# Kernel optimization log

Measured on AMD Instinct MI355X. Metric: run time of the kernel, lower is better.

The kernel has to match this reference:

```python
import jax, jax.numpy as jnp
import numpy as np

D_MODEL = 96
D_STATE = 16
D_INNER = 192   # expand * d_model
DT_RANK = 6     # ceil(96/16)
D_DEPTH_OUT = 1024  # (64/2)*(64/2)
BATCH, HH, WW = 2, 64, 64


def silu(v):
    return v * jax.nn.sigmoid(v)


def setup_inputs() -> dict:
    key = jax.random.key(0)
    ks = jax.random.split(key, 10)
    f = jnp.float32
    x = jax.random.normal(ks[0], (BATCH, HH, WW, D_MODEL), f)
    in_proj_w = jax.random.normal(ks[1], (2 * D_INNER, D_MODEL), f) * 0.02
    conv2d_w = jax.random.normal(ks[2], (D_INNER, 1, 3, 3), f) * 0.1  # depthwise, groups=D_INNER
    conv2d_b = jnp.zeros((D_INNER,), f)
    depth_conv_w = jax.random.normal(ks[3], (D_INNER, 1, 3, 3), f) * 0.1  # depthwise, stride 2
    depth_conv_b = jnp.zeros((D_INNER,), f)
    depth_fc_w = jax.random.normal(ks[4], (D_INNER, D_DEPTH_OUT), f) * 0.02
    depth_fc_b = jnp.zeros((D_INNER,), f)
    x_proj_w = jax.random.normal(ks[5], (DT_RANK + 2 * D_STATE, D_INNER), f) * 0.02
    dt_init_std = DT_RANK ** (-0.5)
    dt_projs_w = jax.random.uniform(ks[6], (D_INNER, DT_RANK), f, -dt_init_std, dt_init_std)
    # inverse-softplus of dt ~ U(log 1e-3, log 0.1)
    dt = jnp.exp(jax.random.uniform(ks[7], (D_INNER,), f) * (np.log(0.1) - np.log(0.001)) + np.log(0.001))
    dt = jnp.clip(dt, 1e-4, None)
    dt_projs_b = dt + jnp.log(-jnp.expm1(-dt))
    A_logs = jnp.log(jnp.tile(jnp.arange(1, D_STATE + 1, dtype=f)[None, :], (D_INNER, 1)))
    Ds = jnp.ones((D_INNER,), f)
    out_norm_w = jnp.ones((D_INNER,), f)
    out_norm_b = jnp.zeros((D_INNER,), f)
    out_proj_w = jax.random.normal(ks[8], (D_MODEL, D_INNER), f) * 0.02
    return dict(x=x, in_proj_w=in_proj_w, conv2d_w=conv2d_w, conv2d_b=conv2d_b,
                depth_conv_w=depth_conv_w, depth_conv_b=depth_conv_b,
                depth_fc_w=depth_fc_w, depth_fc_b=depth_fc_b, x_proj_w=x_proj_w,
                dt_projs_w=dt_projs_w, dt_projs_b=dt_projs_b, A_logs=A_logs, Ds=Ds,
                out_norm_w=out_norm_w, out_norm_b=out_norm_b, out_proj_w=out_proj_w)


def _selective_scan(u, delta, A, Bm, Cm, D, delta_bias):
    # u, delta: [B, D, L]; A: [D, N]; Bm, Cm: [B, N, L]; D: [D]; delta_bias: [D]
    delta = jax.nn.softplus(delta + delta_bias[None, :, None])
    dA = jnp.exp(jnp.einsum('bdl,dn->lbdn', delta, A))          # [L,B,D,N]
    dBu = jnp.einsum('bdl,bnl,bdl->lbdn', delta, Bm, u)          # [L,B,D,N]
    Ct = jnp.transpose(Cm, (2, 0, 1))                            # [L,B,N]
    h0 = jnp.zeros(dA.shape[1:], u.dtype)

    def step(h, inp):
        a, b, c = inp
        h = a * h + b                                            # S6 recurrence
        return h, jnp.einsum('bdn,bn->bd', h, c)

    _, ys = jax.lax.scan(step, h0, (dA, dBu, Ct))                # ys: [L,B,D]
    y = jnp.transpose(ys, (1, 2, 0))                             # [B,D,L]
    return y + D[None, :, None] * u


def _forward(x, in_proj_w, conv2d_w, conv2d_b, depth_conv_w, depth_conv_b,
             depth_fc_w, depth_fc_b, x_proj_w, dt_projs_w, dt_projs_b,
             A_logs, Ds, out_norm_w, out_norm_b, out_proj_w):
    B, H, W, _ = x.shape
    Di, N, R = D_INNER, D_STATE, DT_RANK
    dn = ('NCHW', 'OIHW', 'NCHW')
    xz = x @ in_proj_w.T
    x1, z = jnp.split(xz, 2, axis=-1)
    xc = jnp.transpose(x1, (0, 3, 1, 2))                         # [B,Di,H,W]
    xc = jax.lax.conv_general_dilated(xc, conv2d_w, (1, 1), [(1, 1), (1, 1)],
                                      dimension_numbers=dn, feature_group_count=Di)
    xc = silu(xc + conv2d_b[None, :, None, None])
    dxc = jax.lax.conv_general_dilated(xc, depth_conv_w, (2, 2), [(1, 1), (1, 1)],
                                       dimension_numbers=dn, feature_group_count=Di)
    dxc = dxc + depth_conv_b[None, :, None, None]                # [B,Di,H/2,W/2]
    dx = dxc.reshape(B, Di, -1)                                  # [B,Di,1024]
    dx = dx @ depth_fc_w.T + depth_fc_b                          # [B,Di,Di]
    dx = silu(jnp.transpose(dx, (0, 2, 1)))                      # [B,Di,CC], CC=Di
    L = H * W
    CC = dx.shape[-1]
    xs = jnp.concatenate([dx, xc.reshape(B, Di, L)], axis=-1)    # mode='head': [B,Di,LL]
    x_dbl = jnp.einsum('bdl,cd->bcl', xs, x_proj_w)
    dts, Bm, Cm = x_dbl[:, :R], x_dbl[:, R:R + N], x_dbl[:, R + N:]
    dts = jnp.einsum('brl,dr->bdl', dts, dt_projs_w)
    A = -jnp.exp(A_logs)
    y = _selective_scan(xs, dts, A, Bm, Cm, Ds, dt_projs_b)
    y = y[..., CC:]                                              # drop depth tokens (head mode)
    y = jnp.transpose(y, (0, 2, 1)).reshape(B, H, W, Di)
    mu = jnp.mean(y, axis=-1, keepdims=True)
    var = jnp.var(y, axis=-1, keepdims=True)
    y = (y - mu) * jax.lax.rsqrt(var + 1e-5) * out_norm_w + out_norm_b
    y = y * silu(z)
    return y @ out_proj_w.T


def reference(x, in_proj_w, conv2d_w, conv2d_b, depth_conv_w, depth_conv_b,
              depth_fc_w, depth_fc_b, x_proj_w, dt_projs_w, dt_projs_b,
              A_logs, Ds, out_norm_w, out_norm_b, out_proj_w):
    return _forward(x, in_proj_w, conv2d_w, conv2d_b, depth_conv_w, depth_conv_b,
                    depth_fc_w, depth_fc_b, x_proj_w, dt_projs_w, dt_projs_b,
                    A_logs, Ds, out_norm_w, out_norm_b, out_proj_w)
```

## Files before the change

kernel.cpp:

```cpp
#include <hip/hip_runtime.h>
#include <hip/hip_bf16.h>

typedef __hip_bfloat16 bf16;

#define BATCH 2
#define DM 96
#define DI 192
#define LSP 4096
#define LD 192
#define LTOT 4288
#define NST 16
#define RK 6
#define DFC 1024
#define CLEN 64
#define NCH 67
#define XR 16

__device__ __forceinline__ float b2f(bf16 v) { return __bfloat162float(v); }
__device__ __forceinline__ float silu_f(float x) { return x / (1.f + __expf(-x)); }
__device__ __forceinline__ float softplus_f(float x) { return x > 20.f ? x : log1pf(__expf(x)); }

__device__ __forceinline__ int is_f32(const void* alog) {
    return ((const unsigned int*)alog)[0] == 0u;
}
__device__ __forceinline__ float LDI(const void* p, int i, int f32m) {
    return f32m ? ((const float*)p)[i] : __bfloat162float(((const bf16*)p)[i]);
}
__device__ __forceinline__ void unpack2(unsigned int u, float* o) {
    o[0] = __uint_as_float(u << 16);
    o[1] = __uint_as_float(u & 0xffff0000u);
}

__global__ __launch_bounds__(768) void k_inproj(const void* __restrict__ x, const void* __restrict__ ipw,
                                                const void* __restrict__ alog,
                                                float* __restrict__ x1, float* __restrict__ z) {
    __shared__ uint4 sxr[384];
    const int f32m = is_f32(alog);
    int t = threadIdx.x;
    int col = t >> 1;
    int kh = t & 1;
    int row0 = blockIdx.x * 16;
    float wr[48];
    if (f32m) {
        const float4* wp = (const float4*)((const float*)ipw + col * 96 + kh * 48);
        #pragma unroll
        for (int i = 0; i < 12; i++) {
            float4 v = wp[i];
            wr[4*i] = v.x; wr[4*i+1] = v.y; wr[4*i+2] = v.z; wr[4*i+3] = v.w;
        }
        if (t < 384) sxr[t] = ((const uint4*)((const float*)x + row0 * 96))[t];
        __syncthreads();
        for (int r = 0; r < 16; r++) {
            const uint4* xr = &sxr[r * 24 + kh * 12];
            float acc = 0.f;
            #pragma unroll
            for (int i = 0; i < 12; i++) {
                uint4 u = xr[i];
                acc += __uint_as_float(u.x) * wr[4*i]   + __uint_as_float(u.y) * wr[4*i+1]
                     + __uint_as_float(u.z) * wr[4*i+2] + __uint_as_float(u.w) * wr[4*i+3];
            }
            acc += __shfl_xor(acc, 1);
            if (kh == 0) {
                int row = row0 + r;
                if (col < DI) x1[row * DI + col] = acc;
                else          z[row * DI + (col - DI)] = acc;
            }
        }
    } else {
        const uint4* wp = (const uint4*)((const bf16*)ipw + col * 96 + kh * 48);
        #pragma unroll
        for (int i = 0; i < 6; i++) {
            uint4 v = wp[i];
            unpack2(v.x, &wr[8*i]);   unpack2(v.y, &wr[8*i+2]);
            unpack2(v.z, &wr[8*i+4]); unpack2(v.w, &wr[8*i+6]);
        }
        if (t < 192) sxr[t] = ((const uint4*)((const bf16*)x + row0 * 96))[t];
        __syncthreads();
        for (int r = 0; r < 16; r++) {
            const uint4* xr = &sxr[r * 12 + kh * 6];
            float acc = 0.f;
            #pragma unroll
            for (int i = 0; i < 6; i++) {
                uint4 xv = xr[i];
                float xf8[8];
                unpack2(xv.x, &xf8[0]); unpack2(xv.y, &xf8[2]);
                unpack2(xv.z, &xf8[4]); unpack2(xv.w, &xf8[6]);
                #pragma unroll
                for (int j = 0; j < 8; j++) acc += xf8[j] * wr[8*i + j];
            }
            acc += __shfl_xor(acc, 1);
            if (kh == 0) {
                int row = row0 + r;
                if (col < DI) x1[row * DI + col] = acc;
                else          z[row * DI + (col - DI)] = acc;
            }
        }
    }
}

__global__ __launch_bounds__(192) void k_conv1(const float* __restrict__ x1, const void* __restrict__ cw,
                                               const void* __restrict__ cb, float* __restrict__ xs,
                                               const void* __restrict__ alog) {
    const int f32m = is_f32(alog);
    int d = threadIdx.x;
    int blk = blockIdx.x;
    int b = blk >> 12, l = blk & 4095;
    int h = l >> 6, w_ = l & 63;
    float acc = LDI(cb, d, f32m);
    #pragma unroll
    for (int dh = 0; dh < 3; dh++) {
        int hh = h + dh - 1;
        if ((unsigned)hh >= 64u) continue;
        #pragma unroll
        for (int dw = 0; dw < 3; dw++) {
            int ww = w_ + dw - 1;
            if ((unsigned)ww >= 64u) continue;
            acc += x1[((b << 12) + (hh << 6) + ww) * DI + d] * LDI(cw, d * 9 + dh * 3 + dw, f32m);
        }
    }
    xs[(b * LTOT + LD + l) * DI + d] = silu_f(acc);
}

__global__ __launch_bounds__(192) void k_conv2(const float* __restrict__ xs, const void* __restrict__ dw,
                                               const void* __restrict__ db, float* __restrict__ dxc,
                                               const void* __restrict__ alog) {
    const int f32m = is_f32(alog);
    int d = threadIdx.x;
    int blk = blockIdx.x;
    int b = blk >> 10, lp = blk & 1023;
    int hp = lp >> 5, wp = lp & 31;
    float acc = LDI(db, d, f32m);
    #pragma unroll
    for (int dh = 0; dh < 3; dh++) {
        int h = 2 * hp + dh - 1;
        if ((unsigned)h >= 64u) continue;
        #pragma unroll
        for (int dw_ = 0; dw_ < 3; dw_++) {
            int w_ = 2 * wp + dw_ - 1;
            if ((unsigned)w_ >= 64u) continue;
            acc += xs[(b * LTOT + LD + (h << 6) + w_) * DI + d] * LDI(dw, d * 9 + dh * 3 + dw_, f32m);
        }
    }
    dxc[(b * DFC + lp) * DI + d] = acc;
}

__global__ __launch_bounds__(192) void k_dfc(const float* __restrict__ dxc, const void* __restrict__ fw,
                                             float* __restrict__ part, const void* __restrict__ alog) {
    __shared__ float sfw[4 * 128];
    const int f32m = is_f32(alog);
    int t = threadIdx.x;
    int blk = blockIdx.x;
    int p = blk / 96;
    int rem = blk - p * 96;
    int b   = rem / 48;
    int ch0 = (rem % 48) * 4;
    int k0  = p * 128;
    for (int idx = t; idx < 4 * 128; idx += 192)
        sfw[idx] = LDI(fw, (ch0 + (idx >> 7)) * DFC + k0 + (idx & 127), f32m);
    __syncthreads();
    float a0 = 0.f, a1 = 0.f, a2 = 0.f, a3 = 0.f;
    #pragma unroll 8
    for (int k = 0; k < 128; k++) {
        float dv = dxc[(b * DFC + k0 + k) * DI + t];
        a0 += dv * sfw[k];
        a1 += dv * sfw[128 + k];
        a2 += dv * sfw[256 + k];
        a3 += dv * sfw[384 + k];
    }
    int ob = ((p * 2 + b) * 192 + t) * DI + ch0;
    *(float4*)&part[ob] = make_float4(a0, a1, a2, a3);
}

__global__ __launch_bounds__(256) void k_xdbl(const float* __restrict__ xs_r, float* __restrict__ xs_w,
                                              const float* __restrict__ part, const void* __restrict__ fb,
                                              const void* __restrict__ xpw,
                                              float* __restrict__ BCb, float* __restrict__ dts,
                                              const void* __restrict__ alog) {
    __shared__ float sw[38 * 196];
    __shared__ float srow[XR][196];
    const int f32m = is_f32(alog);
    int t = threadIdx.x;
    for (int c = t >> 3; c < 38; c += 32) {
        int seg = (t & 7) * 24;
        for (int k = seg; k < seg + 24; k++) sw[c * 196 + k] = LDI(xpw, c * DI + k, f32m);
    }
    int row0 = blockIdx.x * XR;
    int bb = row0 >= LTOT ? 1 : 0;
    int depth = (row0 - bb * LTOT) < LD;
    for (int idx = t; idx < XR * DI; idx += 256) {
        int row = idx / DI, k = idx - row * DI;
        int grow = row0 + row;
        float v;
        if (depth) {
            int tok = grow - bb * LTOT;
            int o = (bb * 192 + tok) * DI + k;
            v = 0.f;
            #pragma unroll
            for (int p = 0; p < 8; p++) v += part[o + p * 73728];
            v = silu_f(v + LDI(fb, k, f32m));
            xs_w[grow * DI + k] = v;
        } else {
            v = xs_r[grow * DI + k];
        }
        srow[row][k] = v;
    }
    __syncthreads();
    int r = t & 15, cg = t >> 4;
    float a0 = 0.f, a1 = 0.f, a2 = 0.f;
    const float4* w0 = (const float4*)&sw[cg * 196];
    const float4* w1 = (const float4*)&sw[(cg + 16) * 196];
    const float4* w2 = (const float4*)&sw[(cg < 6 ? cg + 32 : cg) * 196];
    const float4* xr = (const float4*)&srow[r][0];
    #pragma unroll 4
    for (int k = 0; k < 48; k++) {
        float4 xv = xr[k], v0 = w0[k], v1 = w1[k], v2 = w2[k];
        a0 += xv.x * v0.x + xv.y * v0.y + xv.z * v0.z + xv.w * v0.w;
        a1 += xv.x * v1.x + xv.y * v1.y + xv.z * v1.z + xv.w * v1.w;
        a2 += xv.x * v2.x + xv.y * v2.y + xv.z * v2.z + xv.w * v2.w;
    }
    int grow = row0 + r;
    if (cg < 6) dts[grow * 6 + cg] = a0;
    else        BCb[grow * 32 + (cg - 6)] = a0;
    BCb[grow * 32 + (cg + 10)] = a1;
    if (cg < 6) BCb[grow * 32 + (cg + 26)] = a2;
}

__device__ __forceinline__ void scan_stage(const float* __restrict__ dts, const float* __restrict__ xs,
                                           const float* __restrict__ BCb, const void* __restrict__ dtw,
                                           const void* __restrict__ dtb, int f32m,
                                           int bL, int l0, int d0, int t,
                                           float* su, float* sbc, float* sdel,
                                           float* sdts, float* sdwb) {
    {
        int e = t * 4;
        int i = e >> 4, dd = e & 15;
        *(float4*)&su[e] = *(const float4*)&xs[(bL + l0 + i) * DI + d0 + dd];
    }
    #pragma unroll
    for (int q = 0; q < 2; q++) {
        int e = (t + q * 256) * 4;
        int i = e >> 5, c = e & 31;
        *(float4*)&sbc[e] = *(const float4*)&BCb[(bL + l0 + i) * 32 + c];
    }
    for (int idx = t; idx < CLEN * RK; idx += 256) sdts[idx] = dts[(bL + l0) * RK + idx];
    if (t < 96)            sdwb[t] = LDI(dtw, (d0 + t / 6) * RK + (t % 6), f32m);
    else if (t < 112)      sdwb[t] = LDI(dtb, d0 + (t - 96), f32m);
    __syncthreads();
    {
        int e = t * 4;
        int i = e >> 4, dl = e & 15;
        #pragma unroll
        for (int q = 0; q < 4; q++) {
            int dlq = dl + q;
            float dv = sdwb[96 + dlq];
            #pragma unroll
            for (int r2 = 0; r2 < RK; r2++) dv += sdts[i * RK + r2] * sdwb[dlq * RK + r2];
            sdel[e + q] = softplus_f(dv);
        }
    }
    __syncthreads();
}

__global__ __launch_bounds__(256) void k_scan1(const float* __restrict__ dts, const float* __restrict__ xs,
                                               const float* __restrict__ BCb, const void* __restrict__ dtw,
                                               const void* __restrict__ dtb, const void* __restrict__ alog,
                                               float* __restrict__ Af, float* __restrict__ hf) {
    __shared__ float su[CLEN * 16];
    __shared__ float sbc[CLEN * 32];
    __shared__ float sdel[CLEN * 16];
    __shared__ float sdts[CLEN * RK];
    __shared__ float sdwb[112];
    const int f32m = is_f32(alog);
    int t = threadIdx.x;
    int beta = blockIdx.x;
    int b = beta / (12 * NCH);
    int rem = beta - b * (12 * NCH);
    int dblk = rem / NCH, ch = rem - dblk * NCH;
    int d0 = dblk * 16, l0 = ch * CLEN;
    int bL = b * LTOT;
    scan_stage(dts, xs, BCb, dtw, dtb, f32m, bL, l0, d0, t, su, sbc, sdel, sdts, sdwb);
    int dloc = t >> 4, n = t & 15;
    int d = d0 + dloc;
    float A = -__expf(LDI(alog, d * NST + n, f32m));
    float h = 0.f, ap = 1.f;
    #pragma unroll 4
    for (int i = 0; i < CLEN; i++) {
        float dt = sdel[(i << 4) | dloc];
        float u  = su[(i << 4) | dloc];
        float Bv = sbc[(i << 5) | n];
        float a = __expf(dt * A);
        h = a * h + dt * Bv * u;
        ap *= a;
    }
    int o = ((b * DI + d) * NCH + ch) * NST + n;
    Af[o] = ap;
    hf[o] = h;
}

__global__ __launch_bounds__(256) void k_scan3(const float* __restrict__ dts, const float* __restrict__ xs,
                                               const float* __restrict__ BCb, const void* __restrict__ dtw,
                                               const void* __restrict__ dtb, const void* __restrict__ alog,
                                               const void* __restrict__ Dsv,
                                               const float* __restrict__ Af, const float* __restrict__ hf,
                                               float* __restrict__ y) {
    __shared__ float su[CLEN * 16];
    __shared__ float sbc[CLEN * 32];
    __shared__ float sdel[CLEN * 16];
    __shared__ float sdts[CLEN * RK];
    __shared__ float sdwb[112];
    const int f32m = is_f32(alog);
    int t = threadIdx.x;
    int beta = blockIdx.x;
    int b = beta / (12 * NCH);
    int rem = beta - b * (12 * NCH);
    int dblk = rem / NCH, ch = rem - dblk * NCH;
    int d0 = dblk * 16, l0 = ch * CLEN;
    int bL = b * LTOT;
    scan_stage(dts, xs, BCb, dtw, dtb, f32m, bL, l0, d0, t, su, sbc, sdel, sdts, sdwb);
    int dloc = t >> 4, n = t & 15;
    int d = d0 + dloc;
    float A = -__expf(LDI(alog, d * NST + n, f32m));
    float Dv = LDI(Dsv, d, f32m);
    int base = ((b * DI + d) * NCH) * NST + n;
    float h = 0.f;
    for (int c = 0; c < ch; c++) {
        int oo = base + c * NST;
        h = Af[oo] * h + hf[oo];
    }
    for (int i = 0; i < CLEN; i++) {
        float dt = sdel[(i << 4) | dloc];
        float u  = su[(i << 4) | dloc];
        float Bv = sbc[(i << 5) | n];
        float Cv = sbc[(i << 5) | 16 | n];
        float a = __expf(dt * A);
        h = a * h + dt * Bv * u;
        float yv = h * Cv;
        #pragma unroll
        for (int m = 8; m; m >>= 1) yv += __shfl_xor(yv, m, 16);
        int l = l0 + i;
        if (n == 0 && l >= LD) y[(b * LSP + (l - LD)) * DI + d] = yv + Dv * u;
    }
}

__global__ __launch_bounds__(384) void k_out(const float* __restrict__ y, const float* __restrict__ z,
                                             const void* __restrict__ nw, const void* __restrict__ nb,
                                             const void* __restrict__ opw, void* __restrict__ out,
                                             const void* __restrict__ alog) {
    __shared__ float sg[2][DI];
    __shared__ float sred[2][2][3];
    const int f32m = is_f32(alog);
    int t = threadIdx.x;
    int m = t >> 2, kh = t & 3;
    float wr[48];
    if (f32m) {
        const float4* wp = (const float4*)((const float*)opw + m * DI + kh * 48);
        #pragma unroll
        for (int i = 0; i < 12; i++) {
            float4 v = wp[i];
            wr[4*i] = v.x; wr[4*i+1] = v.y; wr[4*i+2] = v.z; wr[4*i+3] = v.w;
        }
    } else {
        const uint4* wp = (const uint4*)((const bf16*)opw + m * DI + kh * 48);
        #pragma unroll
        for (int i = 0; i < 6; i++) {
            uint4 v = wp[i];
            unpack2(v.x, &wr[8*i]);   unpack2(v.y, &wr[8*i+2]);
            unpack2(v.z, &wr[8*i+4]); unpack2(v.w, &wr[8*i+6]);
        }
    }
    float nwv = 0.f, nbv = 0.f;
    if (t < DI) { nwv = LDI(nw, t, f32m); nbv = LDI(nb, t, f32m); }
    int wv_ = t >> 6;
    int row0 = blockIdx.x * 16;
    for (int pr = 0; pr < 8; pr++) {
        int r0 = row0 + pr * 2, r1 = r0 + 1;
        float y0 = 0.f, z0 = 0.f, y1 = 0.f, z1 = 0.f;
        if (t < DI) {
            y0 = y[r0 * DI + t]; z0 = z[r0 * DI + t];
            y1 = y[r1 * DI + t]; z1 = z[r1 * DI + t];
            float s0 = y0, q0 = y0 * y0, s1 = y1, q1 = y1 * y1;
            #pragma unroll
            for (int off = 32; off; off >>= 1) {
                s0 += __shfl_xor(s0, off); q0 += __shfl_xor(q0, off);
                s1 += __shfl_xor(s1, off); q1 += __shfl_xor(q1, off);
            }
            if ((t & 63) == 0) {
                sred[0][0][wv_] = s0; sred[0][1][wv_] = q0;
                sred[1][0][wv_] = s1; sred[1][1][wv_] = q1;
            }
        }
        __syncthreads();
        if (t < DI) {
            float S0  = sred[0][0][0] + sred[0][0][1] + sred[0][0][2];
            float Q0  = sred[0][1][0] + sred[0][1][1] + sred[0][1][2];
            float S1  = sred[1][0][0] + sred[1][0][1] + sred[1][0][2];
            float Q1  = sred[1][1][0] + sred[1][1][1] + sred[1][1][2];
            float mu0 = S0 * (1.f / 192.f), var0 = Q0 * (1.f / 192.f) - mu0 * mu0;
            float mu1 = S1 * (1.f / 192.f), var1 = Q1 * (1.f / 192.f) - mu1 * mu1;
            float g0 = (y0 - mu0) * rsqrtf(var0 + 1e-5f) * nwv + nbv;
            g0 *= z0 / (1.f + __expf(-z0));
            float g1 = (y1 - mu1) * rsqrtf(var1 + 1e-5f) * nwv + nbv;
            g1 *= z1 / (1.f + __expf(-z1));
            sg[0][t] = g0;
            sg[1][t] = g1;
        }
        __syncthreads();
        const float* g0p = &sg[0][kh * 48];
        const float* g1p = &sg[1][kh * 48];
        float a0 = 0.f, a1 = 0.f;
        #pragma unroll
        for (int j = 0; j < 48; j++) {
            a0 += g0p[j] * wr[j];
            a1 += g1p[j] * wr[j];
        }
        a0 += __shfl_xor(a0, 1); a0 += __shfl_xor(a0, 2);
        a1 += __shfl_xor(a1, 1); a1 += __shfl_xor(a1, 2);
        if (kh == 0) {
            if (f32m) {
                ((float*)out)[r0 * DM + m] = a0;
                ((float*)out)[r1 * DM + m] = a1;
            } else {
                ((bf16*)out)[r0 * DM + m] = __float2bfloat16(a0);
                ((bf16*)out)[r1 * DM + m] = __float2bfloat16(a1);
            }
        }
    }
}

extern "C" void kernel_launch(void* const* d_in, const int* in_sizes, int n_in,
                              void* d_out, int out_size, void* d_ws, size_t ws_size,
                              hipStream_t stream) {
    (void)in_sizes; (void)n_in; (void)out_size; (void)ws_size;
    const void* x    = d_in[0];
    const void* ipw  = d_in[1];
    const void* c1w  = d_in[2];
    const void* c1b  = d_in[3];
    const void* c2w  = d_in[4];
    const void* c2b  = d_in[5];
    const void* fcw  = d_in[6];
    const void* fcb  = d_in[7];
    const void* xpw  = d_in[8];
    const void* dtw  = d_in[9];
    const void* dtb  = d_in[10];
    const void* alog = d_in[11];
    const void* Dsv  = d_in[12];
    const void* nw   = d_in[13];
    const void* nb   = d_in[14];
    const void* opw  = d_in[15];

    float* ws  = (float*)d_ws;
    float* x1  = ws;
    float* z   = x1  + BATCH * LSP * DI;
    float* xs  = z   + BATCH * LSP * DI;
    float* dxc = xs  + BATCH * LTOT * DI;
    float* BCb = dxc + BATCH * DFC * DI;
    float* dts = BCb + BATCH * LTOT * 32;
    float* Af  = dts + BATCH * LTOT * RK;
    float* hf  = Af  + BATCH * DI * NCH * NST;
    float* part = x1;
    float* y    = x1;

    k_inproj<<<dim3(512), dim3(768), 0, stream>>>(x, ipw, alog, x1, z);
    k_conv1 <<<dim3(BATCH * LSP), dim3(DI), 0, stream>>>(x1, c1w, c1b, xs, alog);
    k_conv2 <<<dim3(BATCH * DFC), dim3(DI), 0, stream>>>(xs, c2w, c2b, dxc, alog);
    k_dfc   <<<dim3(768), dim3(DI), 0, stream>>>(dxc, fcw, part, alog);
    k_xdbl  <<<dim3(536), dim3(256), 0, stream>>>(xs, xs, part, fcb, xpw, BCb, dts, alog);
    k_scan1 <<<dim3(BATCH * 12 * NCH), dim3(256), 0, stream>>>(dts, xs, BCb, dtw, dtb, alog, Af, hf);
    k_scan3 <<<dim3(BATCH * 12 * NCH), dim3(256), 0, stream>>>(dts, xs, BCb, dtw, dtb, alog, Dsv, Af, hf, y);
    k_out   <<<dim3(512), dim3(384), 0, stream>>>(y, z, nw, nb, opw, d_out, alog);
}
```

Baseline: 236.1 us.

## Tile conv1 over 8 columns, pack chunk carries as float2, overlap carry prefix with staging

The depthwise 3x3 conv now has each block compute 8 horizontally adjacent outputs from a register window of 3x10 inputs. This reuses input loads across neighbouring outputs and cuts the grid from 8192 to 1024 blocks. The chunk summaries are stored as interleaved float2 (A-product, h) in chunk-major order, so the carry prefix in scan3 reads coalesced 8-byte values. scan3 also runs that prefix loop before the first barrier to overlap it with shared-memory staging, and scan1 loads only the B half of the B/C buffer. The cost is fewer blocks for conv1 and more registers per thread.

```diff
diff --git a/kernel.cpp b/kernel.cpp
--- a/kernel.cpp
+++ b/kernel.cpp
@@ -15,6 +15,7 @@
 #define CLEN 64
 #define NCH 67
 #define XR 16
+#define NG  (BATCH * DI * NST)
 
 __device__ __forceinline__ float b2f(bf16 v) { return __bfloat162float(v); }
 __device__ __forceinline__ float silu_f(float x) { return x / (1.f + __expf(-x)); }
@@ -104,21 +105,34 @@
     const int f32m = is_f32(alog);
     int d = threadIdx.x;
     int blk = blockIdx.x;
-    int b = blk >> 12, l = blk & 4095;
-    int h = l >> 6, w_ = l & 63;
-    float acc = LDI(cb, d, f32m);
+    int b = blk >> 9;
+    int rest = blk & 511;
+    int h = rest >> 3, w0 = (rest & 7) * 8;
+    float wgt[9];
+    #pragma unroll
+    for (int i = 0; i < 9; i++) wgt[i] = LDI(cw, d * 9 + i, f32m);
+    float bias = LDI(cb, d, f32m);
+    float val[3][10];
     #pragma unroll
     for (int dh = 0; dh < 3; dh++) {
         int hh = h + dh - 1;
-        if ((unsigned)hh >= 64u) continue;
-        #pragma unroll
-        for (int dw = 0; dw < 3; dw++) {
-            int ww = w_ + dw - 1;
-            if ((unsigned)ww >= 64u) continue;
-            acc += x1[((b << 12) + (hh << 6) + ww) * DI + d] * LDI(cw, d * 9 + dh * 3 + dw, f32m);
-        }
-    }
-    xs[(b * LTOT + LD + l) * DI + d] = silu_f(acc);
+        #pragma unroll
+        for (int j = 0; j < 10; j++) {
+            int ww = w0 + j - 1;
+            val[dh][j] = ((unsigned)hh < 64u && (unsigned)ww < 64u)
+                       ? x1[((b << 12) + (hh << 6) + ww) * DI + d] : 0.f;
+        }
+    }
+    #pragma unroll
+    for (int i = 0; i < 8; i++) {
+        float acc = bias;
+        #pragma unroll
+        for (int dh = 0; dh < 3; dh++)
+            #pragma unroll
+            for (int dw = 0; dw < 3; dw++)
+                acc += val[dh][i + dw] * wgt[dh * 3 + dw];
+        xs[(b * LTOT + LD + (h << 6) + w0 + i) * DI + d] = silu_f(acc);
+    }
 }
 
 __global__ __launch_bounds__(192) void k_conv2(const float* __restrict__ xs, const void* __restrict__ dw,
@@ -225,48 +239,25 @@
     if (cg < 6) BCb[grow * 32 + (cg + 26)] = a2;
 }
 
-__device__ __forceinline__ void scan_stage(const float* __restrict__ dts, const float* __restrict__ xs,
-                                           const float* __restrict__ BCb, const void* __restrict__ dtw,
-                                           const void* __restrict__ dtb, int f32m,
-                                           int bL, int l0, int d0, int t,
-                                           float* su, float* sbc, float* sdel,
-                                           float* sdts, float* sdwb) {
-    {
-        int e = t * 4;
-        int i = e >> 4, dd = e & 15;
-        *(float4*)&su[e] = *(const float4*)&xs[(bL + l0 + i) * DI + d0 + dd];
-    }
-    #pragma unroll
-    for (int q = 0; q < 2; q++) {
-        int e = (t + q * 256) * 4;
-        int i = e >> 5, c = e & 31;
-        *(float4*)&sbc[e] = *(const float4*)&BCb[(bL + l0 + i) * 32 + c];
-    }
-    for (int idx = t; idx < CLEN * RK; idx += 256) sdts[idx] = dts[(bL + l0) * RK + idx];
-    if (t < 96)            sdwb[t] = LDI(dtw, (d0 + t / 6) * RK + (t % 6), f32m);
-    else if (t < 112)      sdwb[t] = LDI(dtb, d0 + (t - 96), f32m);
-    __syncthreads();
-    {
-        int e = t * 4;
-        int i = e >> 4, dl = e & 15;
-        #pragma unroll
-        for (int q = 0; q < 4; q++) {
-            int dlq = dl + q;
-            float dv = sdwb[96 + dlq];
-            #pragma unroll
-            for (int r2 = 0; r2 < RK; r2++) dv += sdts[i * RK + r2] * sdwb[dlq * RK + r2];
-            sdel[e + q] = softplus_f(dv);
-        }
-    }
-    __syncthreads();
+__device__ __forceinline__ void delta_block(const float* sdts, const float* sdwb, float* sdel, int t) {
+    int e = t * 4;
+    int i = e >> 4, dl = e & 15;
+    #pragma unroll
+    for (int q = 0; q < 4; q++) {
+        int dlq = dl + q;
+        float dv = sdwb[96 + dlq];
+        #pragma unroll
+        for (int r2 = 0; r2 < RK; r2++) dv += sdts[i * RK + r2] * sdwb[dlq * RK + r2];
+        sdel[e + q] = softplus_f(dv);
+    }
 }
 
 __global__ __launch_bounds__(256) void k_scan1(const float* __restrict__ dts, const float* __restrict__ xs,
                                                const float* __restrict__ BCb, const void* __restrict__ dtw,
                                                const void* __restrict__ dtb, const void* __restrict__ alog,
-                                               float* __restrict__ Af, float* __restrict__ hf) {
+                                               float2* __restrict__ AH) {
     __shared__ float su[CLEN * 16];
-    __shared__ float sbc[CLEN * 32];
+    __shared__ float sB[CLEN * 16];
     __shared__ float sdel[CLEN * 16];
     __shared__ float sdts[CLEN * RK];
     __shared__ float sdwb[112];
@@ -278,7 +269,18 @@
     int dblk = rem / NCH, ch = rem - dblk * NCH;
     int d0 = dblk * 16, l0 = ch * CLEN;
     int bL = b * LTOT;
-    scan_stage(dts, xs, BCb, dtw, dtb, f32m, bL, l0, d0, t, su, sbc, sdel, sdts, sdwb);
+    {
+        int e = t * 4;
+        int i = e >> 4, dd = e & 15;
+        *(float4*)&su[e] = *(const float4*)&xs[(bL + l0 + i) * DI + d0 + dd];
+        *(float4*)&sB[e] = *(const float4*)&BCb[(bL + l0 + i) * 32 + dd];
+    }
+    for (int idx = t; idx < CLEN * RK; idx += 256) sdts[idx] = dts[(bL + l0) * RK + idx];
+    if (t < 96)            sdwb[t] = LDI(dtw, (d0 + t / 6) * RK + (t % 6), f32m);
+    else if (t < 112)      sdwb[t] = LDI(dtb, d0 + (t - 96), f32m);
+    __syncthreads();
+    delta_block(sdts, sdwb, sdel, t);
+    __syncthreads();
     int dloc = t >> 4, n = t & 15;
     int d = d0 + dloc;
     float A = -__expf(LDI(alog, d * NST + n, f32m));
@@ -287,21 +289,19 @@
     for (int i = 0; i < CLEN; i++) {
         float dt = sdel[(i << 4) | dloc];
         float u  = su[(i << 4) | dloc];
-        float Bv = sbc[(i << 5) | n];
+        float Bv = sB[(i << 4) | n];
         float a = __expf(dt * A);
         h = a * h + dt * Bv * u;
         ap *= a;
     }
-    int o = ((b * DI + d) * NCH + ch) * NST + n;
-    Af[o] = ap;
-    hf[o] = h;
+    int g = ((b * DI + d) * NST) + n;
+    AH[ch * NG + g] = make_float2(ap, h);
 }
 
 __global__ __launch_bounds__(256) void k_scan3(const float* __restrict__ dts, const float* __restrict__ xs,
                                                const float* __restrict__ BCb, const void* __restrict__ dtw,
                                                const void* __restrict__ dtb, const void* __restrict__ alog,
-                                               const void* __restrict__ Dsv,
-                                               const float* __restrict__ Af, const float* __restrict__ hf,
+                                               const void* __restrict__ Dsv, const float2* __restrict__ AH,
                                                float* __restrict__ y) {
     __shared__ float su[CLEN * 16];
     __shared__ float sbc[CLEN * 32];
@@ -316,17 +316,33 @@
     int dblk = rem / NCH, ch = rem - dblk * NCH;
     int d0 = dblk * 16, l0 = ch * CLEN;
     int bL = b * LTOT;
-    scan_stage(dts, xs, BCb, dtw, dtb, f32m, bL, l0, d0, t, su, sbc, sdel, sdts, sdwb);
+    {
+        int e = t * 4;
+        int i = e >> 4, dd = e & 15;
+        *(float4*)&su[e] = *(const float4*)&xs[(bL + l0 + i) * DI + d0 + dd];
+    }
+    #pragma unroll
+    for (int q = 0; q < 2; q++) {
+        int e = (t + q * 256) * 4;
+        int i = e >> 5, c = e & 31;
+        *(float4*)&sbc[e] = *(const float4*)&BCb[(bL + l0 + i) * 32 + c];
+    }
+    for (int idx = t; idx < CLEN * RK; idx += 256) sdts[idx] = dts[(bL + l0) * RK + idx];
+    if (t < 96)            sdwb[t] = LDI(dtw, (d0 + t / 6) * RK + (t % 6), f32m);
+    else if (t < 112)      sdwb[t] = LDI(dtb, d0 + (t - 96), f32m);
     int dloc = t >> 4, n = t & 15;
     int d = d0 + dloc;
+    int g = ((b * DI + d) * NST) + n;
+    float h = 0.f;
+    for (int c = 0; c < ch; c++) {
+        float2 v = AH[c * NG + g];
+        h = v.x * h + v.y;
+    }
+    __syncthreads();
+    delta_block(sdts, sdwb, sdel, t);
+    __syncthreads();
     float A = -__expf(LDI(alog, d * NST + n, f32m));
     float Dv = LDI(Dsv, d, f32m);
-    int base = ((b * DI + d) * NCH) * NST + n;
-    float h = 0.f;
-    for (int c = 0; c < ch; c++) {
-        int oo = base + c * NST;
-        h = Af[oo] * h + hf[oo];
-    }
     for (int i = 0; i < CLEN; i++) {
         float dt = sdel[(i << 4) | dloc];
         float u  = su[(i << 4) | dloc];
@@ -455,17 +471,16 @@
     float* dxc = xs  + BATCH * LTOT * DI;
     float* BCb = dxc + BATCH * DFC * DI;
     float* dts = BCb + BATCH * LTOT * 32;
-    float* Af  = dts + BATCH * LTOT * RK;
-    float* hf  = Af  + BATCH * DI * NCH * NST;
+    float2* AH = (float2*)(dts + BATCH * LTOT * RK);
     float* part = x1;
     float* y    = x1;
 
     k_inproj<<<dim3(512), dim3(768), 0, stream>>>(x, ipw, alog, x1, z);
-    k_conv1 <<<dim3(BATCH * LSP), dim3(DI), 0, stream>>>(x1, c1w, c1b, xs, alog);
+    k_conv1 <<<dim3(1024), dim3(DI), 0, stream>>>(x1, c1w, c1b, xs, alog);
     k_conv2 <<<dim3(BATCH * DFC), dim3(DI), 0, stream>>>(xs, c2w, c2b, dxc, alog);
     k_dfc   <<<dim3(768), dim3(DI), 0, stream>>>(dxc, fcw, part, alog);
     k_xdbl  <<<dim3(536), dim3(256), 0, stream>>>(xs, xs, part, fcb, xpw, BCb, dts, alog);
-    k_scan1 <<<dim3(BATCH * 12 * NCH), dim3(256), 0, stream>>>(dts, xs, BCb, dtw, dtb, alog, Af, hf);
-    k_scan3 <<<dim3(BATCH * 12 * NCH), dim3(256), 0, stream>>>(dts, xs, BCb, dtw, dtb, alog, Dsv, Af, hf, y);
+    k_scan1 <<<dim3(BATCH * 12 * NCH), dim3(256), 0, stream>>>(dts, xs, BCb, dtw, dtb, alog, AH);
+    k_scan3 <<<dim3(BATCH * 12 * NCH), dim3(256), 0, stream>>>(dts, xs, BCb, dtw, dtb, alog, Dsv, AH, y);
     k_out   <<<dim3(512), dim3(384), 0, stream>>>(y, z, nw, nb, opw, d_out, alog);
 }
```

Result: faster. 225.5 us (-4.5%).
